# Kernel tuning notes

Hardware: AMD Instinct MI355X
Metric: run time of the kernel (lower is better)

The kernel has to match this reference:

```python
import jax, jax.numpy as jnp
import numpy as np

DIM = 1024
NUM_HEADS = 16
HEAD_DIM = DIM // NUM_HEADS

def setup_inputs() -> dict:
    key = jax.random.key(0)
    ks = jax.random.split(key, 9)
    s = 1.0 / np.sqrt(DIM)
    x = jax.random.normal(ks[0], (4, 1024, DIM), dtype=jnp.float32)
    Wq = jax.random.uniform(ks[1], (DIM, DIM), jnp.float32, -s, s)
    bq = jax.random.uniform(ks[2], (DIM,), jnp.float32, -s, s)
    Wk = jax.random.uniform(ks[3], (DIM, DIM), jnp.float32, -s, s)
    bk = jax.random.uniform(ks[4], (DIM,), jnp.float32, -s, s)
    Wv = jax.random.uniform(ks[5], (DIM, DIM), jnp.float32, -s, s)
    bv = jax.random.uniform(ks[6], (DIM,), jnp.float32, -s, s)
    Wp = jax.random.uniform(ks[7], (DIM, DIM), jnp.float32, -s, s)
    bp = jax.random.uniform(ks[8], (DIM,), jnp.float32, -s, s)
    return {"x": x, "Wq": Wq, "bq": bq, "Wk": Wk, "bk": bk, "Wv": Wv, "bv": bv, "Wp": Wp, "bp": bp}

def reference(x, Wq, bq, Wk, bk, Wv, bv, Wp, bp):
    B, S, D = x.shape
    H, Hd = NUM_HEADS, HEAD_DIM
    # linear projections (torch Linear: y = x @ W^T + b)
    q = (x @ Wq.T + bq).reshape(B, S, H, Hd).transpose(0, 2, 1, 3)  # [B,H,S,Hd]
    k = (x @ Wk.T + bk).reshape(B, S, H, Hd).transpose(0, 2, 1, 3)
    v = (x @ Wv.T + bv).reshape(B, S, H, Hd).transpose(0, 2, 1, 3)
    score = jnp.einsum("bhsd,bhtd->bhst", q, k) / jnp.sqrt(jnp.float32(Hd))
    attn = jax.nn.softmax(score, axis=-1)  # dropout p=0 -> identity
    wa = jnp.einsum("bhst,bhtd->bhsd", attn, v)  # [B,H,S,Hd]
    wa = wa.transpose(0, 2, 1, 3).reshape(B, S, D)
    out = wa @ Wp.T + bp
    return out
```

## Files before the change

kernel.cpp:

```cpp
#include <hip/hip_runtime.h>

typedef unsigned short u16;
typedef unsigned int   u32;
typedef __attribute__((ext_vector_type(8))) short  short8;
typedef __attribute__((ext_vector_type(8))) __bf16 bf16x8;
typedef __attribute__((ext_vector_type(4))) float  f32x4;

__device__ __forceinline__ u16 f2bf(float f){
  u32 u = __builtin_bit_cast(u32, f);
  u32 r = (u + 0x7FFFu + ((u >> 16) & 1u)) >> 16;
  return (u16)r;
}

__device__ __forceinline__ f32x4 mfma16(short8 a, short8 b, f32x4 c){
  return __builtin_amdgcn_mfma_f32_16x16x32_bf16(
      __builtin_bit_cast(bf16x8, a), __builtin_bit_cast(bf16x8, b), c, 0, 0, 0);
}

__device__ __forceinline__ void gl_lds16(const void* g, void* l){
  __builtin_amdgcn_global_load_lds(
      (const __attribute__((address_space(1))) u32*)g,
      (__attribute__((address_space(3))) u32*)l, 16, 0, 0);
}

#define CQ 0.18033688011112042f

__global__ void cvt_all(const float* __restrict__ x,  const float* __restrict__ Wq,
                        const float* __restrict__ Wk, const float* __restrict__ Wv,
                        const float* __restrict__ Wp,
                        u16* __restrict__ xb, u16* __restrict__ wqkv,
                        u16* __restrict__ wpb){
  int id = blockIdx.x;
  const float* src; u16* dst; int off;
  if (id < 4096){ src = x; dst = xb; off = id << 8; }
  else {
    int t = id - 4096; int w = t >> 10; int o = t & 1023;
    src = (w==0) ? Wq : (w==1) ? Wk : (w==2) ? Wv : Wp;
    dst = (w==3) ? wpb : wqkv + (size_t)w * 1048576;
    off = o << 8;
  }
  int i = off + threadIdx.x;
  float4 v = reinterpret_cast<const float4*>(src)[i];
  ushort4 u;
  u.x = f2bf(v.x); u.y = f2bf(v.y); u.z = f2bf(v.z); u.w = f2bf(v.w);
  reinterpret_cast<ushort4*>(dst)[i] = u;
}

template<int MODE, int BN>
__global__ __launch_bounds__(256) void gemm_bt(
    const u16* __restrict__ A, const u16* __restrict__ B,
    const float* __restrict__ bq, const float* __restrict__ bk,
    const float* __restrict__ bv,
    u16* __restrict__ Oq, u16* __restrict__ Ok, u16* __restrict__ Ovt,
    float* __restrict__ Of, int M, int N, int K)
{
  constexpr int NB = BN / 32;
  __shared__ u16 As[2][128*32];
  __shared__ u16 Bs[2][BN*32];
  const int tid  = threadIdx.x;
  const int wid  = tid >> 6, lane = tid & 63;

  int gx = gridDim.x;
  int lin = blockIdx.y * gx + blockIdx.x;
  int cpx = (gx * gridDim.y) >> 3;
  int lin2 = (lin & 7) * cpx + (lin >> 3);
  const int m0 = (lin2 / gx) * 128, n0 = (lin2 % gx) * BN;
  const int wr = (wid >> 1) * 64, wc = (wid & 1) * (BN/2);

  f32x4 acc[4][NB] = {};
  const int nk = K >> 5;

  auto stage = [&](int buf, int k0){
    #pragma unroll
    for (int ii = 0; ii < 2; ++ii){
      int i = wid * 2 + ii;
      int row = i * 16 + (lane >> 2);
      gl_lds16(A + (size_t)(m0 + row) * K + k0 + (lane & 3) * 8,
               (char*)&As[buf][0] + i * 1024);
    }
    #pragma unroll
    for (int ii = 0; ii < BN/64; ++ii){
      int i = wid * (BN/64) + ii;
      int row = i * 16 + (lane >> 2);
      gl_lds16(B + (size_t)(n0 + row) * K + k0 + (lane & 3) * 8,
               (char*)&Bs[buf][0] + i * 1024);
    }
  };

  stage(0, 0);
  __syncthreads();
  for (int kt = 0; kt < nk; ++kt){
    int cur = kt & 1;
    if (kt + 1 < nk) stage(cur ^ 1, (kt + 1) << 5);
    short8 a[4], b[NB];
    #pragma unroll
    for (int mb = 0; mb < 4; ++mb)
      a[mb] = *(const short8*)&As[cur][(wr + mb*16 + (lane & 15)) * 32 + (lane >> 4) * 8];
    #pragma unroll
    for (int nb = 0; nb < NB; ++nb)
      b[nb] = *(const short8*)&Bs[cur][(wc + nb*16 + (lane & 15)) * 32 + (lane >> 4) * 8];
    #pragma unroll
    for (int mb = 0; mb < 4; ++mb)
      #pragma unroll
      for (int nb = 0; nb < NB; ++nb)
        acc[mb][nb] = mfma16(a[mb], b[nb], acc[mb][nb]);
    __syncthreads();
  }

  const int region = n0 >> 10;
  #pragma unroll
  for (int mb = 0; mb < 4; ++mb){
    int gr0 = m0 + wr + mb * 16 + (lane >> 4) * 4;
    #pragma unroll
    for (int nb = 0; nb < NB; ++nb){
      int gc = n0 + wc + nb * 16 + (lane & 15);
      if (MODE == 1){
        float cbv = bq[gc];
        #pragma unroll
        for (int r = 0; r < 4; ++r)
          Of[(size_t)(gr0 + r) * N + gc] = acc[mb][nb][r] + cbv;
      } else {
        int lc = gc & 1023;
        if (region < 2){
          u16* O = region == 0 ? Oq : Ok;
          float cbv = region == 0 ? bq[lc] : bk[lc];
          float s   = region == 0 ? CQ : 1.0f;
          #pragma unroll
          for (int r = 0; r < 4; ++r)
            O[(size_t)(gr0 + r) * 1024 + lc] = f2bf((acc[mb][nb][r] + cbv) * s);
        } else {
          float cbv = bv[lc];
          ushort4 o;
          o.x = f2bf(acc[mb][nb][0] + cbv);
          o.y = f2bf(acc[mb][nb][1] + cbv);
          o.z = f2bf(acc[mb][nb][2] + cbv);
          o.w = f2bf(acc[mb][nb][3] + cbv);
          *reinterpret_cast<ushort4*>(&Ovt[(size_t)lc * 4096 + gr0]) = o;
        }
      }
    }
  }
}

__global__ __launch_bounds__(256) void attn_kernel(
    const u16* __restrict__ Q, const u16* __restrict__ Kb,
    const u16* __restrict__ VT, u16* __restrict__ WA)
{
  __shared__ u16 Ks [2][64*64];
  __shared__ u16 VTs[2][64*64];
  __shared__ u16 Ps [4][16*64];

  const int tid = threadIdx.x, wid = tid >> 6, lane = tid & 63;
  const int g = lane >> 4, c = lane & 15;

  const int xcd = blockIdx.x & 7, idx = blockIdx.x >> 3;
  const int bh = xcd * 8 + (idx >> 2), qg = idx & 3;
  const int h = bh & 15, b = bh >> 4;

  const u16* Qbase = Q + (size_t)(b*1024 + qg*256 + wid*16 + c)*1024 + h*64 + g*8;
  short8 qf[4][2];
  #pragma unroll
  for (int s = 0; s < 4; ++s){
    qf[s][0] = *(const short8*)(Qbase + (size_t)s*64*1024);
    qf[s][1] = *(const short8*)(Qbase + (size_t)s*64*1024 + 32);
  }

  const char* kg[2]; const char* vg[2];
  #pragma unroll
  for (int ii = 0; ii < 2; ++ii){
    int i  = wid*2 + ii;
    int p0 = i*1024 + lane*16;
    int t  = p0 >> 7;
    int cb2 = (p0 & 127) ^ ((t & 7) << 4);
    kg[ii] = (const char*)(Kb + (size_t)(b*1024 + t)*1024 + h*64) + cb2;
    vg[ii] = (const char*)(VT + (size_t)(h*64 + t)*4096 + b*1024) + cb2;
  }

  auto stage = [&](int buf){
    #pragma unroll
    for (int ii = 0; ii < 2; ++ii){
      int i = wid*2 + ii;
      gl_lds16(kg[ii], (char*)&Ks[buf][0]  + i*1024);
      gl_lds16(vg[ii], (char*)&VTs[buf][0] + i*1024);
      kg[ii] += 64*1024*2;
      vg[ii] += 64*2;
    }
  };

  char* Psw = (char*)&Ps[wid][0];
  float lsum[4][4] = {};
  f32x4 acc[4][4] = {};

  stage(0);
  __syncthreads();

  for (int kt = 0; kt < 16; ++kt){
    const int cur = kt & 1;
    if (kt < 15) stage(cur ^ 1);
    const char* Kc = (const char*)&Ks[cur][0];
    const char* Vc = (const char*)&VTs[cur][0];

    #pragma unroll
    for (int s = 0; s < 4; ++s){
      f32x4 sc[4];
      __builtin_amdgcn_s_setprio(1);
      #pragma unroll
      for (int jb = 0; jb < 4; ++jb){
        int trow = jb*16 + c;
        int swz  = (trow & 7) << 4;
        short8 k0 = *(const short8*)(Kc + trow*128 + ((g*16) ^ swz));
        short8 k1 = *(const short8*)(Kc + trow*128 + ((64 + g*16) ^ swz));
        sc[jb] = mfma16(qf[s][0], k0, f32x4{0.f,0.f,0.f,0.f});
        sc[jb] = mfma16(qf[s][1], k1, sc[jb]);
      }
      __builtin_amdgcn_s_setprio(0);

      #pragma unroll
      for (int jb = 0; jb < 4; ++jb){
        int blk = ((jb ^ g) & 3) << 5;
        #pragma unroll
        for (int r = 0; r < 4; ++r){
          float p = exp2f(sc[jb][r]);
          lsum[s][r] += p;
          *(u16*)(Psw + (4*g + r)*128 + blk + c*2) =
              __builtin_bit_cast(u16, (__bf16)p);
        }
      }
      asm volatile("s_waitcnt lgkmcnt(0)" ::: "memory");
      __builtin_amdgcn_sched_barrier(0);

      __builtin_amdgcn_s_setprio(1);
      #pragma unroll
      for (int tf = 0; tf < 2; ++tf){
        int k2  = (tf*32 + g*8) * 2;
        int jbr = k2 >> 5;
        short8 pf = *(const short8*)(Psw + c*128 + ((((jbr ^ (c >> 2)) & 3) << 5) | (k2 & 31)));
        #pragma unroll
        for (int cb = 0; cb < 4; ++cb){
          int d = cb*16 + c;
          short8 vf = *(const short8*)(Vc + d*128 + (k2 ^ ((d & 7) << 4)));
          acc[s][cb] = mfma16(pf, vf, acc[s][cb]);
        }
      }
      __builtin_amdgcn_s_setprio(0);
    }
    __syncthreads();
  }

  #pragma unroll
  for (int s = 0; s < 4; ++s)
    #pragma unroll
    for (int r = 0; r < 4; ++r){
      float v = lsum[s][r];
      v += __shfl_xor(v, 1); v += __shfl_xor(v, 2);
      v += __shfl_xor(v, 4); v += __shfl_xor(v, 8);
      lsum[s][r] = 1.0f / v;
    }

  #pragma unroll
  for (int s = 0; s < 4; ++s){
    const int m = b*1024 + qg*256 + s*64 + wid*16 + g*4;
    #pragma unroll
    for (int cb = 0; cb < 4; ++cb){
      int gc = h*64 + cb*16 + c;
      #pragma unroll
      for (int r = 0; r < 4; ++r)
        WA[(size_t)(m + r)*1024 + gc] = f2bf(acc[s][cb][r] * lsum[s][r]);
    }
  }
}

extern "C" void kernel_launch(void* const* d_in, const int* in_sizes, int n_in,
                              void* d_out, int out_size, void* d_ws, size_t ws_size,
                              hipStream_t stream)
{
  (void)in_sizes; (void)n_in; (void)out_size; (void)ws_size;
  const float* x  = (const float*)d_in[0];
  const float* Wq = (const float*)d_in[1];
  const float* bq = (const float*)d_in[2];
  const float* Wk = (const float*)d_in[3];
  const float* bk = (const float*)d_in[4];
  const float* Wv = (const float*)d_in[5];
  const float* bv = (const float*)d_in[6];
  const float* Wp = (const float*)d_in[7];
  const float* bp = (const float*)d_in[8];
  float* out = (float*)d_out;

  char* ws = (char*)d_ws;
  const size_t MB = 1u << 20;
  u16* xb   = (u16*)(ws +  0*MB);
  u16* wqkv = (u16*)(ws +  8*MB);
  u16* wpb  = (u16*)(ws + 14*MB);
  u16* Qb   = (u16*)(ws + 16*MB);
  u16* Kb   = (u16*)(ws + 24*MB);
  u16* VTb  = (u16*)(ws + 32*MB);
  u16* WAb  = (u16*)(ws + 40*MB);

  cvt_all<<<8192, 256, 0, stream>>>(x, Wq, Wk, Wv, Wp, xb, wqkv, wpb);

  gemm_bt<0,128><<<dim3(24,32), 256, 0, stream>>>(xb, wqkv, bq, bk, bv,
                                                  Qb, Kb, VTb, nullptr, 4096, 3072, 1024);

  attn_kernel<<<256, 256, 0, stream>>>(Qb, Kb, VTb, WAb);

  gemm_bt<1,64><<<dim3(16,32), 256, 0, stream>>>(WAb, wpb, bp, bp, bp,
                                                 nullptr, nullptr, nullptr, out, 4096, 1024, 1024);
}
```

Measured before the change: 202.6 us.

## Split attention blocks to 64 query rows and raise grid to 1024 blocks

```diff
diff --git a/kernel.cpp b/kernel.cpp
--- a/kernel.cpp
+++ b/kernel.cpp
@@ -142,7 +142,7 @@
   }
 }
 
-__global__ __launch_bounds__(256) void attn_kernel(
+__global__ __launch_bounds__(256, 4) void attn_kernel(
     const u16* __restrict__ Q, const u16* __restrict__ Kb,
     const u16* __restrict__ VT, u16* __restrict__ WA)
 {
@@ -154,15 +154,30 @@
   const int g = lane >> 4, c = lane & 15;
 
   const int xcd = blockIdx.x & 7, idx = blockIdx.x >> 3;
-  const int bh = xcd * 8 + (idx >> 2), qg = idx & 3;
+  const int bh = xcd * 8 + (idx >> 4), qt = idx & 15;
   const int h = bh & 15, b = bh >> 4;
 
-  const u16* Qbase = Q + (size_t)(b*1024 + qg*256 + wid*16 + c)*1024 + h*64 + g*8;
-  short8 qf[4][2];
-  #pragma unroll
-  for (int s = 0; s < 4; ++s){
-    qf[s][0] = *(const short8*)(Qbase + (size_t)s*64*1024);
-    qf[s][1] = *(const short8*)(Qbase + (size_t)s*64*1024 + 32);
+  const int qr = b*1024 + qt*64 + wid*16 + c;
+  short8 qf0 = *(const short8*)&Q[(size_t)qr*1024 + h*64 +      g*8];
+  short8 qf1 = *(const short8*)&Q[(size_t)qr*1024 + h*64 + 32 + g*8];
+
+  int koff[4][2], voff[2][4], poff[2], pwb2[4];
+  #pragma unroll
+  for (int jb = 0; jb < 4; ++jb){
+    int trow = jb*16 + c, swz = (trow & 7) << 4;
+    koff[jb][0] = trow*128 + ((      g*16) ^ swz);
+    koff[jb][1] = trow*128 + ((64 +  g*16) ^ swz);
+    pwb2[jb]    = g*512 + c*2 + (((jb ^ g) & 3) << 5);
+  }
+  #pragma unroll
+  for (int tf = 0; tf < 2; ++tf){
+    int k2 = tf*64 + g*16;
+    #pragma unroll
+    for (int cb = 0; cb < 4; ++cb){
+      int d = cb*16 + c;
+      voff[tf][cb] = d*128 + (k2 ^ ((d & 7) << 4));
+    }
+    poff[tf] = c*128 + (((((k2 >> 5) ^ (c >> 2)) & 3) << 5) | (k2 & 31));
   }
 
   const char* kg[2]; const char* vg[2];
@@ -188,85 +203,74 @@
   };
 
   char* Psw = (char*)&Ps[wid][0];
-  float lsum[4][4] = {};
-  f32x4 acc[4][4] = {};
+  float lsum[4] = {0.f,0.f,0.f,0.f};
+  f32x4 acc[4] = {};
+
+#define COMPUTE_TILE(BUF)                                                      \
+  {                                                                            \
+    const char* Kc = (const char*)&Ks[BUF][0];                                 \
+    const char* Vc = (const char*)&VTs[BUF][0];                                \
+    f32x4 sc[4];                                                               \
+    __builtin_amdgcn_s_setprio(1);                                             \
+    _Pragma("unroll")                                                          \
+    for (int jb = 0; jb < 4; ++jb){                                            \
+      short8 k0 = *(const short8*)(Kc + koff[jb][0]);                          \
+      short8 k1 = *(const short8*)(Kc + koff[jb][1]);                          \
+      sc[jb] = mfma16(qf0, k0, f32x4{0.f,0.f,0.f,0.f});                        \
+      sc[jb] = mfma16(qf1, k1, sc[jb]);                                        \
+    }                                                                          \
+    __builtin_amdgcn_s_setprio(0);                                             \
+    _Pragma("unroll")                                                          \
+    for (int jb = 0; jb < 4; ++jb){                                            \
+      _Pragma("unroll")                                                        \
+      for (int r = 0; r < 4; ++r){                                             \
+        float p = exp2f(sc[jb][r]);                                            \
+        lsum[r] += p;                                                          \
+        *(u16*)(Psw + pwb2[jb] + r*128) = __builtin_bit_cast(u16, (__bf16)p);  \
+      }                                                                        \
+    }                                                                          \
+    asm volatile("s_waitcnt lgkmcnt(0)" ::: "memory");                         \
+    __builtin_amdgcn_sched_barrier(0);                                         \
+    __builtin_amdgcn_s_setprio(1);                                             \
+    _Pragma("unroll")                                                          \
+    for (int tf = 0; tf < 2; ++tf){                                            \
+      short8 pf = *(const short8*)(Psw + poff[tf]);                            \
+      _Pragma("unroll")                                                        \
+      for (int cb = 0; cb < 4; ++cb){                                          \
+        short8 vf = *(const short8*)(Vc + voff[tf][cb]);                       \
+        acc[cb] = mfma16(pf, vf, acc[cb]);                                     \
+      }                                                                        \
+    }                                                                          \
+    __builtin_amdgcn_s_setprio(0);                                             \
+  }
 
   stage(0);
   __syncthreads();
-
-  for (int kt = 0; kt < 16; ++kt){
-    const int cur = kt & 1;
-    if (kt < 15) stage(cur ^ 1);
-    const char* Kc = (const char*)&Ks[cur][0];
-    const char* Vc = (const char*)&VTs[cur][0];
-
-    #pragma unroll
-    for (int s = 0; s < 4; ++s){
-      f32x4 sc[4];
-      __builtin_amdgcn_s_setprio(1);
-      #pragma unroll
-      for (int jb = 0; jb < 4; ++jb){
-        int trow = jb*16 + c;
-        int swz  = (trow & 7) << 4;
-        short8 k0 = *(const short8*)(Kc + trow*128 + ((g*16) ^ swz));
-        short8 k1 = *(const short8*)(Kc + trow*128 + ((64 + g*16) ^ swz));
-        sc[jb] = mfma16(qf[s][0], k0, f32x4{0.f,0.f,0.f,0.f});
-        sc[jb] = mfma16(qf[s][1], k1, sc[jb]);
-      }
-      __builtin_amdgcn_s_setprio(0);
-
-      #pragma unroll
-      for (int jb = 0; jb < 4; ++jb){
-        int blk = ((jb ^ g) & 3) << 5;
-        #pragma unroll
-        for (int r = 0; r < 4; ++r){
-          float p = exp2f(sc[jb][r]);
-          lsum[s][r] += p;
-          *(u16*)(Psw + (4*g + r)*128 + blk + c*2) =
-              __builtin_bit_cast(u16, (__bf16)p);
-        }
-      }
-      asm volatile("s_waitcnt lgkmcnt(0)" ::: "memory");
-      __builtin_amdgcn_sched_barrier(0);
-
-      __builtin_amdgcn_s_setprio(1);
-      #pragma unroll
-      for (int tf = 0; tf < 2; ++tf){
-        int k2  = (tf*32 + g*8) * 2;
-        int jbr = k2 >> 5;
-        short8 pf = *(const short8*)(Psw + c*128 + ((((jbr ^ (c >> 2)) & 3) << 5) | (k2 & 31)));
-        #pragma unroll
-        for (int cb = 0; cb < 4; ++cb){
-          int d = cb*16 + c;
-          short8 vf = *(const short8*)(Vc + d*128 + (k2 ^ ((d & 7) << 4)));
-          acc[s][cb] = mfma16(pf, vf, acc[s][cb]);
-        }
-      }
-      __builtin_amdgcn_s_setprio(0);
-    }
+  for (int kt2 = 0; kt2 < 8; ++kt2){
+    stage(1);
+    COMPUTE_TILE(0)
     __syncthreads();
-  }
-
-  #pragma unroll
-  for (int s = 0; s < 4; ++s)
-    #pragma unroll
-    for (int r = 0; r < 4; ++r){
-      float v = lsum[s][r];
-      v += __shfl_xor(v, 1); v += __shfl_xor(v, 2);
-      v += __shfl_xor(v, 4); v += __shfl_xor(v, 8);
-      lsum[s][r] = 1.0f / v;
-    }
-
-  #pragma unroll
-  for (int s = 0; s < 4; ++s){
-    const int m = b*1024 + qg*256 + s*64 + wid*16 + g*4;
-    #pragma unroll
-    for (int cb = 0; cb < 4; ++cb){
-      int gc = h*64 + cb*16 + c;
-      #pragma unroll
-      for (int r = 0; r < 4; ++r)
-        WA[(size_t)(m + r)*1024 + gc] = f2bf(acc[s][cb][r] * lsum[s][r]);
-    }
+    if (kt2 < 7) stage(0);
+    COMPUTE_TILE(1)
+    __syncthreads();
+  }
+#undef COMPUTE_TILE
+
+  #pragma unroll
+  for (int r = 0; r < 4; ++r){
+    float v = lsum[r];
+    v += __shfl_xor(v, 1); v += __shfl_xor(v, 2);
+    v += __shfl_xor(v, 4); v += __shfl_xor(v, 8);
+    lsum[r] = 1.0f / v;
+  }
+
+  const int m = b*1024 + qt*64 + wid*16 + g*4;
+  #pragma unroll
+  for (int cb = 0; cb < 4; ++cb){
+    int gc = h*64 + cb*16 + c;
+    #pragma unroll
+    for (int r = 0; r < 4; ++r)
+      WA[(size_t)(m + r)*1024 + gc] = f2bf(acc[cb][r] * lsum[r]);
   }
 }
 
@@ -301,7 +305,7 @@
   gemm_bt<0,128><<<dim3(24,32), 256, 0, stream>>>(xb, wqkv, bq, bk, bv,
                                                   Qb, Kb, VTb, nullptr, 4096, 3072, 1024);
 
-  attn_kernel<<<256, 256, 0, stream>>>(Qb, Kb, VTb, WAb);
+  attn_kernel<<<1024, 256, 0, stream>>>(Qb, Kb, VTb, WAb);
 
   gemm_bt<1,64><<<dim3(16,32), 256, 0, stream>>>(WAb, wpb, bp, bp, bp,
                                                  nullptr, nullptr, nullptr, out, 4096, 1024, 1024);
```

Result: faster. 181.6 us (-10.4%).
